# Performance work log

Hardware: AMD Instinct MI355X
Metric: run time of the kernel (lower is better)

## Reference

```python
import jax, jax.numpy as jnp
import numpy as np

N = 100000   # nodes
E = 1600000  # edges
D = 128      # input / hidden feature dim
H = 16       # inner GCN bottleneck (gin default hidden_filters=(16,))
C = 40       # num_classes (ogbn-arxiv)
L = 3        # GCN2 layers
EPS = 1e-5   # hk.BatchNorm default eps


def setup_inputs() -> dict:
    key = jax.random.key(0)
    ks = jax.random.split(key, 8)
    x = jax.random.normal(ks[0], (N, D), jnp.float32)
    vals = jax.random.uniform(ks[1], (E,), jnp.float32)
    row = jnp.sort(jax.random.randint(ks[2], (E,), 0, N, jnp.int32))
    col = jax.random.randint(ks[3], (E,), 0, N, jnp.int32)
    W1 = jax.random.normal(ks[4], (L, D, H), jnp.float32) * 0.1
    b1 = jnp.zeros((L, H), jnp.float32)
    W2 = jax.random.normal(ks[5], (L, H, D), jnp.float32) * 0.1
    b2 = jnp.zeros((L, D), jnp.float32)
    gamma = jnp.ones((L, D), jnp.float32)
    beta = jnp.zeros((L, D), jnp.float32)
    W1f = jax.random.normal(ks[6], (D, H), jnp.float32) * 0.1
    b1f = jnp.zeros((H,), jnp.float32)
    W2f = jax.random.normal(ks[7], (H, C), jnp.float32) * 0.1
    b2f = jnp.zeros((C,), jnp.float32)
    return dict(x=x, vals=vals, W1=W1, b1=b1, W2=W2, b2=b2, gamma=gamma,
                beta=beta, W1f=W1f, b1f=b1f, W2f=W2f, b2f=b2f, row=row, col=col)


def spmm(row, col, vals, h):
    # out[i] = sum_{e: row[e]==i} vals[e] * h[col[e]]  (A @ h, A sparse COO)
    return jax.ops.segment_sum(vals[:, None] * h[col], row,
                               num_segments=N, indices_are_sorted=True)


def gcn_block(x, row, col, vals, w1, c1, w2, c2):
    # inner GCN: GraphConv(16) -> relu -> GraphConv(out); dropout_rate=0 -> identity
    h = spmm(row, col, vals, x @ w1) + c1
    h = jax.nn.relu(h)
    return spmm(row, col, vals, h @ w2) + c2


def reference(x, vals, W1, b1, W2, b2, gamma, beta, W1f, b1f, W2f, b2f, row, col):
    for i in range(L):
        h = gcn_block(x, row, col, vals, W1[i], b1[i], W2[i], b2[i])
        # BatchNorm (training mode: batch stats over node axis)
        mean = jnp.mean(h, axis=0)
        var = jnp.mean(jnp.square(h), axis=0) - jnp.square(mean)
        h = (h - mean) * jax.lax.rsqrt(var + EPS) * gamma[i] + beta[i]
        x = jax.nn.relu(h)
    logits = gcn_block(x, row, col, vals, W1f, b1f, W2f, b2f)
    return logits
```

## Files before the change

### kernel.cpp

```cpp
#include <hip/hip_runtime.h>

#define NN 100000
#define NE 1600000
#define DD 128
#define HH 16
#define CC 40
#define LL 3

typedef int   vi4 __attribute__((ext_vector_type(4)));
typedef float vf4 __attribute__((ext_vector_type(4)));

__device__ __forceinline__ float4 f4fma(float s, float4 w, float4 a) {
    a.x = fmaf(s, w.x, a.x); a.y = fmaf(s, w.y, a.y);
    a.z = fmaf(s, w.z, a.z); a.w = fmaf(s, w.w, a.w);
    return a;
}

__device__ __forceinline__ unsigned short f2bf(float f) {
    unsigned u = __float_as_uint(f);
    unsigned r = u + 0x7fffu + ((u >> 16) & 1u);
    return (unsigned short)(r >> 16);
}
__device__ __forceinline__ unsigned pk2(float a, float b) {
    return (unsigned)f2bf(a) | ((unsigned)f2bf(b) << 16);
}
__device__ __forceinline__ float bflo(unsigned u) { return __uint_as_float(u << 16); }
__device__ __forceinline__ float bfhi(unsigned u) { return __uint_as_float(u & 0xffff0000u); }

__device__ __forceinline__ int permW2(int dw) {
    return (dw >> 2) | ((dw & 3) << 3);
}

__global__ void build_rowptr(const int* __restrict__ row, int* __restrict__ rp) {
    int e = blockIdx.x * 256 + threadIdx.x;
    if (e >= NE) return;
    int r1 = row[e];
    int r0 = (e == 0) ? -1 : row[e - 1];
    for (int i = r0 + 1; i <= r1; i++) rp[i] = e;
    if (e == NE - 1) {
        for (int i = r1 + 1; i <= NN; i++) rp[i] = NE;
    }
}

__global__ void zero_buf(float* __restrict__ s, int n) {
    int i = blockIdx.x * 256 + threadIdx.x;
    if (i < n) s[i] = 0.f;
}

__launch_bounds__(256)
__global__ void gemm_dh_reg(const float* __restrict__ X, const float* __restrict__ W,
                            unsigned* __restrict__ Y) {
    __shared__ float4 Ws[DD * 4];
    int t = threadIdx.x;
    for (int i = t; i < DD * 4; i += 256) Ws[i] = ((const float4*)W)[i];
    __syncthreads();
    int n = blockIdx.x * 256 + t;
    if (n >= NN) return;
    const float4* X4 = (const float4*)(X + (size_t)n * DD);
    float4 y0 = {0,0,0,0}, y1 = {0,0,0,0}, y2 = {0,0,0,0}, y3 = {0,0,0,0};
    #pragma unroll 8
    for (int dc = 0; dc < 32; dc++) {
        float4 xv = X4[dc];
        float xs[4] = {xv.x, xv.y, xv.z, xv.w};
        #pragma unroll
        for (int j = 0; j < 4; j++) {
            int d = dc * 4 + j;
            float xj = xs[j];
            y0 = f4fma(xj, Ws[d * 4 + 0], y0);
            y1 = f4fma(xj, Ws[d * 4 + 1], y1);
            y2 = f4fma(xj, Ws[d * 4 + 2], y2);
            y3 = f4fma(xj, Ws[d * 4 + 3], y3);
        }
    }
    uint4 o0 = {pk2(y0.x, y0.y), pk2(y0.z, y0.w), pk2(y1.x, y1.y), pk2(y1.z, y1.w)};
    uint4 o1 = {pk2(y2.x, y2.y), pk2(y2.z, y2.w), pk2(y3.x, y3.y), pk2(y3.z, y3.w)};
    ((uint4*)Y)[(size_t)n * 2]     = o0;
    ((uint4*)Y)[(size_t)n * 2 + 1] = o1;
}

#define FMA_B(vv, g0, g1, g2, g3)                                                      \
    acc.x = fmaf(vv.x, bflo(g0.x), acc.x); acc.y = fmaf(vv.x, bfhi(g0.x), acc.y);      \
    acc.z = fmaf(vv.x, bflo(g0.y), acc.z); acc.w = fmaf(vv.x, bfhi(g0.y), acc.w);      \
    acc.x = fmaf(vv.y, bflo(g1.x), acc.x); acc.y = fmaf(vv.y, bfhi(g1.x), acc.y);      \
    acc.z = fmaf(vv.y, bflo(g1.y), acc.z); acc.w = fmaf(vv.y, bfhi(g1.y), acc.w);      \
    acc.x = fmaf(vv.z, bflo(g2.x), acc.x); acc.y = fmaf(vv.z, bfhi(g2.x), acc.y);      \
    acc.z = fmaf(vv.z, bflo(g2.y), acc.z); acc.w = fmaf(vv.z, bfhi(g2.y), acc.w);      \
    acc.x = fmaf(vv.w, bflo(g3.x), acc.x); acc.y = fmaf(vv.w, bfhi(g3.x), acc.y);      \
    acc.z = fmaf(vv.w, bflo(g3.y), acc.z); acc.w = fmaf(vv.w, bfhi(g3.y), acc.w);

__device__ __forceinline__ void ldc(const int* __restrict__ col,
                                    const float* __restrict__ vals,
                                    int jb, int s, int e, vi4& c, vf4& v) {
    c = *(const vi4*)(col + jb);
    vf4 w = *(const vf4*)(vals + jb);
    int r = jb - s;
    unsigned deg = (unsigned)(e - s);
    v.x = ((unsigned)(r + 0) < deg) ? w.x : 0.f;
    v.y = ((unsigned)(r + 1) < deg) ? w.y : 0.f;
    v.z = ((unsigned)(r + 2) < deg) ? w.z : 0.f;
    v.w = ((unsigned)(r + 3) < deg) ? w.w : 0.f;
}

template <bool RELU, bool BIAS, bool OBF, bool GRAM, bool FINAL>
__launch_bounds__(256)
__global__ void spmm16(const int* __restrict__ rp, const int* __restrict__ col,
                       const float* __restrict__ vals, const unsigned* __restrict__ hin,
                       const float* __restrict__ bias, void* __restrict__ outv,
                       float* __restrict__ GS, const float* __restrict__ Wf,
                       const float* __restrict__ bf, float* __restrict__ outc) {
    __shared__ float2 Wc[FINAL ? HH * 20 : 1];
    __shared__ float2 Bc[FINAL ? 20 : 1];
    if (FINAL) {
        for (int i = threadIdx.x; i < HH * 20; i += 256) Wc[i] = ((const float2*)Wf)[i];
        if (threadIdx.x < 20) Bc[threadIdx.x] = ((const float2*)bf)[threadIdx.x];
    }
    int node = blockIdx.x * 64 + (threadIdx.x >> 2);
    int f = threadIdx.x & 3;
    bool valid = node < NN;
    if (!GRAM && !FINAL && !valid) return;
    float4 acc = {0, 0, 0, 0};
    if (valid) {
        int s = rp[node], e = rp[node + 1];
        const uint2* h2 = (const uint2*)hin;
        int deg = e - s;
        if (deg > 0) {
            int s0 = s & ~3;
            int B = (e - s0 + 3) >> 2;
            vi4 c2, c0, c1; vf4 v0, v1, v2;
            ldc(col, vals, s0, s, e, c0, v0);
            if (B > 1) ldc(col, vals, s0 + 4, s, e, c1, v1);
            else { c1 = c0; v1 = (vf4){0, 0, 0, 0}; }
            if (B > 2) ldc(col, vals, s0 + 8, s, e, c2, v2);
            else { c2 = c1; v2 = (vf4){0, 0, 0, 0}; }
            uint2 gA0 = h2[(size_t)c0.x * 4 + f], gA1 = h2[(size_t)c0.y * 4 + f];
            uint2 gA2 = h2[(size_t)c0.z * 4 + f], gA3 = h2[(size_t)c0.w * 4 + f];
            uint2 gB0 = h2[(size_t)c1.x * 4 + f], gB1 = h2[(size_t)c1.y * 4 + f];
            uint2 gB2 = h2[(size_t)c1.z * 4 + f], gB3 = h2[(size_t)c1.w * 4 + f];
            for (int b = 0; b < B; b++) {
                vi4 c3; vf4 v3;
                if (b + 3 < B) ldc(col, vals, s0 + ((b + 3) << 2), s, e, c3, v3);
                else { c3 = c2; v3 = (vf4){0, 0, 0, 0}; }
                uint2 gC0 = h2[(size_t)c2.x * 4 + f], gC1 = h2[(size_t)c2.y * 4 + f];
                uint2 gC2 = h2[(size_t)c2.z * 4 + f], gC3 = h2[(size_t)c2.w * 4 + f];
                FMA_B(v0, gA0, gA1, gA2, gA3)
                v0 = v1; v1 = v2; v2 = v3; c2 = c3;
                gA0 = gB0; gA1 = gB1; gA2 = gB2; gA3 = gB3;
                gB0 = gC0; gB1 = gC1; gB2 = gC2; gB3 = gC3;
            }
        }
        if (BIAS) {
            float4 b = ((const float4*)bias)[f];
            acc.x += b.x; acc.y += b.y; acc.z += b.z; acc.w += b.w;
        }
        if (RELU) {
            acc.x = fmaxf(acc.x, 0.f); acc.y = fmaxf(acc.y, 0.f);
            acc.z = fmaxf(acc.z, 0.f); acc.w = fmaxf(acc.w, 0.f);
        }
        if (!FINAL) {
            if (OBF) {
                uint2 o = {pk2(acc.x, acc.y), pk2(acc.z, acc.w)};
                ((uint2*)outv)[(size_t)node * 4 + f] = o;
            } else {
                ((float4*)outv)[(size_t)node * 4 + f] = acc;
            }
        }
    }
    if (GRAM) {
        __shared__ float Us[64 * 20];
        int nl = threadIdx.x >> 2;
        float4 z = valid ? acc : (float4){0, 0, 0, 0};
        ((float4*)&Us[nl * 20])[f] = z;
        __syncthreads();
        int k = threadIdx.x & 15, kp = threadIdx.x >> 4;
        float g = 0.f, s = 0.f;
        for (int n = 0; n < 64; n++) {
            float a = Us[n * 20 + k];
            float b = Us[n * 20 + kp];
            g = fmaf(a, b, g);
            s += a;
        }
        float* gs = GS + (blockIdx.x & 7) * 272;
        atomicAdd(&gs[kp * 16 + k], g);
        if (kp == 0) atomicAdd(&gs[256 + k], s);
    }
    if (FINAL) {
        __shared__ float Us[64 * 20];
        int nl = threadIdx.x >> 2;
        ((float4*)&Us[nl * 20])[f] = acc;
        __syncthreads();
        int p = threadIdx.x & 3;
        int onode = blockIdx.x * 64 + (threadIdx.x >> 2);
        if (onode < NN) {
            float u[16];
            #pragma unroll
            for (int k = 0; k < 16; k++) u[k] = Us[(threadIdx.x >> 2) * 20 + k];
            float2 a5[5];
            #pragma unroll
            for (int i = 0; i < 5; i++) a5[i] = Bc[p * 5 + i];
            #pragma unroll
            for (int k = 0; k < 16; k++) {
                float uk = u[k];
                #pragma unroll
                for (int i = 0; i < 5; i++) {
                    float2 w = Wc[k * 20 + p * 5 + i];
                    a5[i].x = fmaf(uk, w.x, a5[i].x);
                    a5[i].y = fmaf(uk, w.y, a5[i].y);
                }
            }
            float2* O = (float2*)(outc + (size_t)onode * CC) + p * 5;
            #pragma unroll
            for (int i = 0; i < 5; i++) O[i] = a5[i];
        }
    }
}

__launch_bounds__(128)
__global__ void bn_prep(const float* __restrict__ GS, const float* __restrict__ W2,
                        const float* __restrict__ b2, const float* __restrict__ gamma,
                        const float* __restrict__ beta, float* __restrict__ SCSH) {
    __shared__ float Gs[272];
    int t = threadIdx.x;
    for (int i = t; i < 272; i += 128) {
        float a = 0.f;
        #pragma unroll
        for (int c = 0; c < 8; c++) a += GS[c * 272 + i];
        Gs[i] = a;
    }
    __syncthreads();
    int d = t;
    float w[16];
    #pragma unroll
    for (int k = 0; k < 16; k++) w[k] = W2[k * DD + d];
    float sdot = 0.f, quad = 0.f;
    #pragma unroll
    for (int k = 0; k < 16; k++) {
        sdot = fmaf(Gs[256 + k], w[k], sdot);
        float vk = 0.f;
        #pragma unroll
        for (int kp = 0; kp < 16; kp++) vk = fmaf(Gs[k * 16 + kp], w[kp], vk);
        quad = fmaf(w[k], vk, quad);
    }
    float b = b2[d];
    float sumH  = sdot + (float)NN * b;
    float sumsq = quad + 2.f * b * sdot + (float)NN * b * b;
    float mean = sumH * (1.f / NN);
    float var  = sumsq * (1.f / NN) - mean * mean;
    float inv  = rsqrtf(var + 1e-5f);
    float gm = gamma[d] * inv;
    SCSH[d] = gm;
    SCSH[128 + d] = (b - mean) * gm + beta[d];
}

__launch_bounds__(256)
__global__ void fused_mid(const float* __restrict__ U, const float* __restrict__ SCSH,
                          const float* __restrict__ W2, const float* __restrict__ W1n,
                          unsigned* __restrict__ Y) {
    __shared__ float4 W2s[HH * 32];
    __shared__ float4 W1s[DD * 4];
    __shared__ float4 SC4[32], SH4[32];
    int t = threadIdx.x;
    for (int i = t; i < HH * 32; i += 256) {
        int k = i >> 5, dw = i & 31;
        W2s[k * 32 + permW2(dw)] = ((const float4*)W2)[i];
    }
    for (int i = t; i < DD * 4; i += 256) {
        int d = i >> 2, q = i & 3;
        W1s[d * 4 + ((q + (d >> 4)) & 3)] = ((const float4*)W1n)[i];
    }
    if (t < 32) SC4[permW2(t)] = ((const float4*)SCSH)[t];
    else if (t < 64) SH4[permW2(t - 32)] = ((const float4*)SCSH)[t];
    __syncthreads();
    int g = t >> 3, p = t & 7;
    int base = blockIdx.x * 64;
    int n[2]; bool v[2];
    #pragma unroll
    for (int i = 0; i < 2; i++) { n[i] = base + i * 32 + g; v[i] = n[i] < NN; }
    float u[2][16];
    #pragma unroll
    for (int i = 0; i < 2; i++) {
        if (v[i]) {
            const float4* up = (const float4*)(U + (size_t)n[i] * HH);
            float4 a = up[0], b = up[1], c = up[2], d = up[3];
            u[i][0]=a.x; u[i][1]=a.y; u[i][2]=a.z; u[i][3]=a.w;
            u[i][4]=b.x; u[i][5]=b.y; u[i][6]=b.z; u[i][7]=b.w;
            u[i][8]=c.x; u[i][9]=c.y; u[i][10]=c.z; u[i][11]=c.w;
            u[i][12]=d.x; u[i][13]=d.y; u[i][14]=d.z; u[i][15]=d.w;
        } else {
            #pragma unroll
            for (int k = 0; k < 16; k++) u[i][k] = 0.f;
        }
    }
    float4 y[2][4];
    #pragma unroll
    for (int i = 0; i < 2; i++)
        #pragma unroll
        for (int q = 0; q < 4; q++) y[i][q] = {0, 0, 0, 0};
    #pragma unroll
    for (int dqi = 0; dqi < 4; dqi++) {
        int rpos = p + (dqi << 3);
        float4 h[2] = {{0,0,0,0},{0,0,0,0}};
        #pragma unroll
        for (int k = 0; k < 16; k++) {
            float4 w = W2s[k * 32 + rpos];
            h[0] = f4fma(u[0][k], w, h[0]);
            h[1] = f4fma(u[1][k], w, h[1]);
        }
        float4 s4 = SC4[rpos], t4 = SH4[rpos];
        #pragma unroll
        for (int i = 0; i < 2; i++) {
            h[i].x = fmaxf(fmaf(h[i].x, s4.x, t4.x), 0.f);
            h[i].y = fmaxf(fmaf(h[i].y, s4.y, t4.y), 0.f);
            h[i].z = fmaxf(fmaf(h[i].z, s4.z, t4.z), 0.f);
            h[i].w = fmaxf(fmaf(h[i].w, s4.w, t4.w), 0.f);
        }
        int dq = (p << 2) + dqi;
        #pragma unroll
        for (int j = 0; j < 4; j++) {
            int d = (dq << 2) + j;
            float4 w0 = W1s[d * 4 + ((0 + p) & 3)];
            float4 w1 = W1s[d * 4 + ((1 + p) & 3)];
            float4 w2 = W1s[d * 4 + ((2 + p) & 3)];
            float4 w3 = W1s[d * 4 + ((3 + p) & 3)];
            float h0 = j == 0 ? h[0].x : j == 1 ? h[0].y : j == 2 ? h[0].z : h[0].w;
            float h1 = j == 0 ? h[1].x : j == 1 ? h[1].y : j == 2 ? h[1].z : h[1].w;
            y[0][0] = f4fma(h0, w0, y[0][0]); y[0][1] = f4fma(h0, w1, y[0][1]);
            y[0][2] = f4fma(h0, w2, y[0][2]); y[0][3] = f4fma(h0, w3, y[0][3]);
            y[1][0] = f4fma(h1, w0, y[1][0]); y[1][1] = f4fma(h1, w1, y[1][1]);
            y[1][2] = f4fma(h1, w2, y[1][2]); y[1][3] = f4fma(h1, w3, y[1][3]);
        }
    }
    float4 ar[4];
    #pragma unroll
    for (int q = 0; q < 4; q++) {
        float4 z0 = y[0][q], z1 = y[1][q];
        z0.x += __shfl_xor(z0.x, 4); z0.y += __shfl_xor(z0.y, 4);
        z0.z += __shfl_xor(z0.z, 4); z0.w += __shfl_xor(z0.w, 4);
        z1.x += __shfl_xor(z1.x, 4); z1.y += __shfl_xor(z1.y, 4);
        z1.z += __shfl_xor(z1.z, 4); z1.w += __shfl_xor(z1.w, 4);
        ar[q].x = (p & 4) ? z1.x : z0.x;
        ar[q].y = (p & 4) ? z1.y : z0.y;
        ar[q].z = (p & 4) ? z1.z : z0.z;
        ar[q].w = (p & 4) ? z1.w : z0.w;
    }
    float4 br[2];
    #pragma unroll
    for (int q = 0; q < 2; q++) {
        float4 z0 = ar[q], z1 = ar[2 + q];
        z0.x += __shfl_xor(z0.x, 2); z0.y += __shfl_xor(z0.y, 2);
        z0.z += __shfl_xor(z0.z, 2); z0.w += __shfl_xor(z0.w, 2);
        z1.x += __shfl_xor(z1.x, 2); z1.y += __shfl_xor(z1.y, 2);
        z1.z += __shfl_xor(z1.z, 2); z1.w += __shfl_xor(z1.w, 2);
        br[q].x = (p & 2) ? z1.x : z0.x;
        br[q].y = (p & 2) ? z1.y : z0.y;
        br[q].z = (p & 2) ? z1.z : z0.z;
        br[q].w = (p & 2) ? z1.w : z0.w;
    }
    float4 c;
    {
        float4 z0 = br[0], z1 = br[1];
        z0.x += __shfl_xor(z0.x, 1); z0.y += __shfl_xor(z0.y, 1);
        z0.z += __shfl_xor(z0.z, 1); z0.w += __shfl_xor(z0.w, 1);
        z1.x += __shfl_xor(z1.x, 1); z1.y += __shfl_xor(z1.y, 1);
        z1.z += __shfl_xor(z1.z, 1); z1.w += __shfl_xor(z1.w, 1);
        c.x = (p & 1) ? z1.x : z0.x;
        c.y = (p & 1) ? z1.y : z0.y;
        c.z = (p & 1) ? z1.z : z0.z;
        c.w = (p & 1) ? z1.w : z0.w;
    }
    bool vv = (p & 4) ? v[1] : v[0];
    int  nn = (p & 4) ? n[1] : n[0];
    int  q  = p & 3;
    if (vv) {
        uint2 o = {pk2(c.x, c.y), pk2(c.z, c.w)};
        ((uint2*)Y)[(size_t)nn * 4 + q] = o;
    }
}

extern "C" void kernel_launch(void* const* d_in, const int* in_sizes, int n_in,
                              void* d_out, int out_size, void* d_ws, size_t ws_size,
                              hipStream_t stream) {
    const float* x     = (const float*)d_in[0];
    const float* vals  = (const float*)d_in[1];
    const float* W1    = (const float*)d_in[2];
    const float* b1    = (const float*)d_in[3];
    const float* W2    = (const float*)d_in[4];
    const float* b2    = (const float*)d_in[5];
    const float* gamma = (const float*)d_in[6];
    const float* beta  = (const float*)d_in[7];
    const float* W1f   = (const float*)d_in[8];
    const float* b1f   = (const float*)d_in[9];
    const float* W2f   = (const float*)d_in[10];
    const float* b2f   = (const float*)d_in[11];
    const int*   row   = (const int*)d_in[12];
    const int*   col   = (const int*)d_in[13];
    float* out = (float*)d_out;

    char* ws = (char*)d_ws;
    size_t off = 0;
    auto alloc = [&](size_t bytes) -> char* {
        char* p = ws + off;
        off += (bytes + 255) / 256 * 256;
        return p;
    };
    int*      rp   = (int*)     alloc((NN + 1) * sizeof(int));
    float*    GSC  = (float*)   alloc((size_t)LL * 8 * 272 * sizeof(float));
    float*    SCSH = (float*)   alloc(256 * sizeof(float));
    unsigned* Yb   = (unsigned*)alloc((size_t)NN * HH * 2);
    unsigned* Tb   = (unsigned*)alloc((size_t)NN * HH * 2);
    float*    U    = (float*)   alloc((size_t)NN * HH * sizeof(float));

    build_rowptr<<<(NE + 255) / 256, 256, 0, stream>>>(row, rp);
    zero_buf<<<(LL * 8 * 272 + 255) / 256, 256, 0, stream>>>(GSC, LL * 8 * 272);

    gemm_dh_reg<<<(NN + 255) / 256, 256, 0, stream>>>(x, W1, Yb);
    for (int l = 0; l < LL; l++) {
        spmm16<true, true, true, false, false><<<(NN + 63) / 64, 256, 0, stream>>>(
            rp, col, vals, Yb, b1 + l * HH, Tb, nullptr, nullptr, nullptr, nullptr);
        spmm16<false, false, false, true, false><<<(NN + 63) / 64, 256, 0, stream>>>(
            rp, col, vals, Tb, nullptr, U, GSC + (size_t)l * 8 * 272, nullptr, nullptr, nullptr);
        bn_prep<<<1, 128, 0, stream>>>(GSC + (size_t)l * 8 * 272, W2 + l * HH * DD,
                                       b2 + l * DD, gamma + l * DD, beta + l * DD, SCSH);
        const float* W1next = (l < LL - 1) ? (W1 + (l + 1) * DD * HH) : W1f;
        fused_mid<<<(NN + 63) / 64, 256, 0, stream>>>(U, SCSH, W2 + l * HH * DD, W1next, Yb);
    }
    spmm16<true, true, true, false, false><<<(NN + 63) / 64, 256, 0, stream>>>(
        rp, col, vals, Yb, b1f, Tb, nullptr, nullptr, nullptr, nullptr);
    spmm16<false, false, false, false, true><<<(NN + 63) / 64, 256, 0, stream>>>(
        rp, col, vals, Tb, nullptr, nullptr, nullptr, W2f, b2f, out);
}
```

Before: 370.5 us.

## Bin nodes by SpMM trip count and process them in permuted order

Adds a preprocessing pass (count, prefix, scatter) that groups nodes into 16 bins by their padded neighbor-chunk trip count and builds a permutation. Each SpMM launch then maps threads to nodes through this permutation, so nodes in the same wavefront have similar degree and fewer lanes sit idle in the edge loop. In exchange it adds several small kernel launches, including a serial per-bin prefix scan over all blocks. Row-pointer reads and output writes also become scattered rather than contiguous.

```diff
diff --git a/kernel.cpp b/kernel.cpp
--- a/kernel.cpp
+++ b/kernel.cpp
@@ -6,6 +6,7 @@
 #define HH 16
 #define CC 40
 #define LL 3
+#define NBINB ((NN + 255) / 256)
 
 typedef int   vi4 __attribute__((ext_vector_type(4)));
 typedef float vf4 __attribute__((ext_vector_type(4)));
@@ -45,6 +46,58 @@
 __global__ void zero_buf(float* __restrict__ s, int n) {
     int i = blockIdx.x * 256 + threadIdx.x;
     if (i < n) s[i] = 0.f;
+}
+
+__device__ __forceinline__ int trip_bin(const int* __restrict__ rp, int n) {
+    int s = rp[n], e = rp[n + 1];
+    return min(15, (e - (s & ~3) + 3) >> 2);
+}
+
+__global__ void bin_count(const int* __restrict__ rp, int* __restrict__ bh,
+                          int* __restrict__ gh) {
+    __shared__ int lh[16];
+    int t = threadIdx.x;
+    if (t < 16) lh[t] = 0;
+    __syncthreads();
+    int n = blockIdx.x * 256 + t;
+    if (n < NN) atomicAdd(&lh[trip_bin(rp, n)], 1);
+    __syncthreads();
+    if (t < 16) {
+        bh[blockIdx.x * 16 + t] = lh[t];
+        atomicAdd(&gh[t], lh[t]);
+    }
+}
+
+__global__ void bin_prefix(const int* __restrict__ gh, const int* __restrict__ bh,
+                           int* __restrict__ bbase) {
+    __shared__ int gbase[16];
+    if (threadIdx.x == 0) {
+        int a = 0;
+        for (int i = 0; i < 16; i++) { gbase[i] = a; a += gh[i]; }
+    }
+    __syncthreads();
+    if (threadIdx.x < 16) {
+        int bin = threadIdx.x;
+        int a = gbase[bin];
+        for (int b = 0; b < NBINB; b++) {
+            bbase[b * 16 + bin] = a;
+            a += bh[b * 16 + bin];
+        }
+    }
+}
+
+__global__ void bin_scatter(const int* __restrict__ rp, const int* __restrict__ bbase,
+                            int* __restrict__ perm) {
+    __shared__ int cnt[16];
+    int t = threadIdx.x;
+    if (t < 16) cnt[t] = 0;
+    __syncthreads();
+    int n = blockIdx.x * 256 + t;
+    if (n < NN) {
+        int B = trip_bin(rp, n);
+        int r = atomicAdd(&cnt[B], 1);
+        perm[bbase[blockIdx.x * 16 + B] + r] = n;
+    }
 }
 
 __launch_bounds__(256)
@@ -107,16 +160,18 @@
                        const float* __restrict__ vals, const unsigned* __restrict__ hin,
                        const float* __restrict__ bias, void* __restrict__ outv,
                        float* __restrict__ GS, const float* __restrict__ Wf,
-                       const float* __restrict__ bf, float* __restrict__ outc) {
+                       const float* __restrict__ bf, float* __restrict__ outc,
+                       const int* __restrict__ perm) {
     __shared__ float2 Wc[FINAL ? HH * 20 : 1];
     __shared__ float2 Bc[FINAL ? 20 : 1];
     if (FINAL) {
         for (int i = threadIdx.x; i < HH * 20; i += 256) Wc[i] = ((const float2*)Wf)[i];
         if (threadIdx.x < 20) Bc[threadIdx.x] = ((const float2*)bf)[threadIdx.x];
     }
-    int node = blockIdx.x * 64 + (threadIdx.x >> 2);
+    int lid = blockIdx.x * 64 + (threadIdx.x >> 2);
     int f = threadIdx.x & 3;
-    bool valid = node < NN;
+    bool valid = lid < NN;
+    int node = valid ? perm[lid] : 0;
     if (!GRAM && !FINAL && !valid) return;
     float4 acc = {0, 0, 0, 0};
     if (valid) {
@@ -189,8 +244,7 @@
         ((float4*)&Us[nl * 20])[f] = acc;
         __syncthreads();
         int p = threadIdx.x & 3;
-        int onode = blockIdx.x * 64 + (threadIdx.x >> 2);
-        if (onode < NN) {
+        if (valid) {
             float u[16];
             #pragma unroll
             for (int k = 0; k < 16; k++) u[k] = Us[(threadIdx.x >> 2) * 20 + k];
@@ -207,7 +261,7 @@
                     a5[i].y = fmaf(uk, w.y, a5[i].y);
                 }
             }
-            float2* O = (float2*)(outc + (size_t)onode * CC) + p * 5;
+            float2* O = (float2*)(outc + (size_t)node * CC) + p * 5;
             #pragma unroll
             for (int i = 0; i < 5; i++) O[i] = a5[i];
         }
@@ -402,29 +456,38 @@
         off += (bytes + 255) / 256 * 256;
         return p;
     };
-    int*      rp   = (int*)     alloc((NN + 1) * sizeof(int));
-    float*    GSC  = (float*)   alloc((size_t)LL * 8 * 272 * sizeof(float));
-    float*    SCSH = (float*)   alloc(256 * sizeof(float));
-    unsigned* Yb   = (unsigned*)alloc((size_t)NN * HH * 2);
-    unsigned* Tb   = (unsigned*)alloc((size_t)NN * HH * 2);
-    float*    U    = (float*)   alloc((size_t)NN * HH * sizeof(float));
+    int*      rp    = (int*)     alloc((NN + 1) * sizeof(int));
+    float*    GSC   = (float*)   alloc((size_t)LL * 8 * 272 * sizeof(float));
+    float*    SCSH  = (float*)   alloc(256 * sizeof(float));
+    unsigned* Yb    = (unsigned*)alloc((size_t)NN * HH * 2);
+    unsigned* Tb    = (unsigned*)alloc((size_t)NN * HH * 2);
+    float*    U     = (float*)   alloc((size_t)NN * HH * sizeof(float));
+    int*      bh    = (int*)     alloc((size_t)NBINB * 16 * sizeof(int));
+    int*      bbase = (int*)     alloc((size_t)NBINB * 16 * sizeof(int));
+    int*      gh    = (int*)     alloc(16 * sizeof(int));
+    int*      perm  = (int*)     alloc((size_t)NN * sizeof(int));
 
     build_rowptr<<<(NE + 255) / 256, 256, 0, stream>>>(row, rp);
     zero_buf<<<(LL * 8 * 272 + 255) / 256, 256, 0, stream>>>(GSC, LL * 8 * 272);
+    zero_buf<<<1, 256, 0, stream>>>((float*)gh, 16);
+
+    bin_count<<<NBINB, 256, 0, stream>>>(rp, bh, gh);
+    bin_prefix<<<1, 256, 0, stream>>>(gh, bh, bbase);
+    bin_scatter<<<NBINB, 256, 0, stream>>>(rp, bbase, perm);
 
     gemm_dh_reg<<<(NN + 255) / 256, 256, 0, stream>>>(x, W1, Yb);
     for (int l = 0; l < LL; l++) {
         spmm16<true, true, true, false, false><<<(NN + 63) / 64, 256, 0, stream>>>(
-            rp, col, vals, Yb, b1 + l * HH, Tb, nullptr, nullptr, nullptr, nullptr);
+            rp, col, vals, Yb, b1 + l * HH, Tb, nullptr, nullptr, nullptr, nullptr, perm);
         spmm16<false, false, false, true, false><<<(NN + 63) / 64, 256, 0, stream>>>(
-            rp, col, vals, Tb, nullptr, U, GSC + (size_t)l * 8 * 272, nullptr, nullptr, nullptr);
+            rp, col, vals, Tb, nullptr, U, GSC + (size_t)l * 8 * 272, nullptr, nullptr, nullptr, perm);
         bn_prep<<<1, 128, 0, stream>>>(GSC + (size_t)l * 8 * 272, W2 + l * HH * DD,
                                        b2 + l * DD, gamma + l * DD, beta + l * DD, SCSH);
         const float* W1next = (l < LL - 1) ? (W1 + (l + 1) * DD * HH) : W1f;
         fused_mid<<<(NN + 63) / 64, 256, 0, stream>>>(U, SCSH, W2 + l * HH * DD, W1next, Yb);
     }
     spmm16<true, true, true, false, false><<<(NN + 63) / 64, 256, 0, stream>>>(
-        rp, col, vals, Yb, b1f, Tb, nullptr, nullptr, nullptr, nullptr);
+        rp, col, vals, Yb, b1f, Tb, nullptr, nullptr, nullptr, nullptr, perm);
     spmm16<false, false, false, false, true><<<(NN + 63) / 64, 256, 0, stream>>>(
-        rp, col, vals, Tb, nullptr, nullptr, nullptr, W2f, b2f, out);
-}
+        rp, col, vals, Tb, nullptr, nullptr, nullptr, W2f, b2f, out, perm);
+}
```

Result: slower. 435.2 us (+17.4%).

## Sort nodes by trip count within each 64-node block and use nontemporal loads for col and vals

Applied to the files above, without the earlier changes.

Adds a local_sort kernel that reorders nodes within each 64-node block by their number of 4-edge chunks. Every spmm16 launch then reads its node index through that permutation, so the lanes of a wavefront handle rows of similar length and spend less time diverging. Loads of col and vals are also made nontemporal, to keep that streamed edge data from evicting the gathered feature rows from cache. The cost is one extra launch, an extra indirection per node, and scattered output writes. The GRAM and non-final paths write U and Tb through the permuted node index in code not shown here, so correctness depends on those writes also using node.

```diff
diff --git a/kernel.cpp b/kernel.cpp
--- a/kernel.cpp
+++ b/kernel.cpp
@@ -45,6 +45,29 @@
 __global__ void zero_buf(float* __restrict__ s, int n) {
     int i = blockIdx.x * 256 + threadIdx.x;
     if (i < n) s[i] = 0.f;
+}
+
+__device__ __forceinline__ int trip_bin(const int* __restrict__ rp, int n) {
+    int s = rp[n], e = rp[n + 1];
+    return (e - (s & ~3) + 3) >> 2;
+}
+
+__global__ void local_sort(const int* __restrict__ rp, int* __restrict__ perm) {
+    __shared__ int Bs[64];
+    int t = threadIdx.x;
+    int base = blockIdx.x * 64;
+    int n = base + t;
+    int B = (n < NN) ? trip_bin(rp, n) : -1;
+    Bs[t] = B;
+    __syncthreads();
+    if (n < NN) {
+        int rank = 0;
+        for (int j = 0; j < 64; j++) {
+            int Bj = Bs[j];
+            rank += (Bj > B) || (Bj == B && j < t);
+        }
+        perm[base + rank] = n;
+    }
 }
 
 __launch_bounds__(256)
@@ -91,8 +114,8 @@
 __device__ __forceinline__ void ldc(const int* __restrict__ col,
                                     const float* __restrict__ vals,
                                     int jb, int s, int e, vi4& c, vf4& v) {
-    c = *(const vi4*)(col + jb);
-    vf4 w = *(const vf4*)(vals + jb);
+    c = __builtin_nontemporal_load((const vi4*)(col + jb));
+    vf4 w = __builtin_nontemporal_load((const vf4*)(vals + jb));
     int r = jb - s;
     unsigned deg = (unsigned)(e - s);
     v.x = ((unsigned)(r + 0) < deg) ? w.x : 0.f;
@@ -107,16 +130,18 @@
                        const float* __restrict__ vals, const unsigned* __restrict__ hin,
                        const float* __restrict__ bias, void* __restrict__ outv,
                        float* __restrict__ GS, const float* __restrict__ Wf,
-                       const float* __restrict__ bf, float* __restrict__ outc) {
+                       const float* __restrict__ bf, float* __restrict__ outc,
+                       const int* __restrict__ perm) {
     __shared__ float2 Wc[FINAL ? HH * 20 : 1];
     __shared__ float2 Bc[FINAL ? 20 : 1];
     if (FINAL) {
         for (int i = threadIdx.x; i < HH * 20; i += 256) Wc[i] = ((const float2*)Wf)[i];
         if (threadIdx.x < 20) Bc[threadIdx.x] = ((const float2*)bf)[threadIdx.x];
     }
-    int node = blockIdx.x * 64 + (threadIdx.x >> 2);
+    int lid = blockIdx.x * 64 + (threadIdx.x >> 2);
     int f = threadIdx.x & 3;
-    bool valid = node < NN;
+    bool valid = lid < NN;
+    int node = valid ? perm[lid] : 0;
     if (!GRAM && !FINAL && !valid) return;
     float4 acc = {0, 0, 0, 0};
     if (valid) {
@@ -189,8 +214,7 @@
         ((float4*)&Us[nl * 20])[f] = acc;
         __syncthreads();
         int p = threadIdx.x & 3;
-        int onode = blockIdx.x * 64 + (threadIdx.x >> 2);
-        if (onode < NN) {
+        if (valid) {
             float u[16];
             #pragma unroll
             for (int k = 0; k < 16; k++) u[k] = Us[(threadIdx.x >> 2) * 20 + k];
@@ -207,7 +231,7 @@
                     a5[i].y = fmaf(uk, w.y, a5[i].y);
                 }
             }
-            float2* O = (float2*)(outc + (size_t)onode * CC) + p * 5;
+            float2* O = (float2*)(outc + (size_t)node * CC) + p * 5;
             #pragma unroll
             for (int i = 0; i < 5; i++) O[i] = a5[i];
         }
@@ -408,23 +432,25 @@
     unsigned* Yb   = (unsigned*)alloc((size_t)NN * HH * 2);
     unsigned* Tb   = (unsigned*)alloc((size_t)NN * HH * 2);
     float*    U    = (float*)   alloc((size_t)NN * HH * sizeof(float));
+    int*      perm = (int*)     alloc((size_t)((NN + 63) / 64 * 64) * sizeof(int));
 
     build_rowptr<<<(NE + 255) / 256, 256, 0, stream>>>(row, rp);
     zero_buf<<<(LL * 8 * 272 + 255) / 256, 256, 0, stream>>>(GSC, LL * 8 * 272);
+    local_sort<<<(NN + 63) / 64, 64, 0, stream>>>(rp, perm);
 
     gemm_dh_reg<<<(NN + 255) / 256, 256, 0, stream>>>(x, W1, Yb);
     for (int l = 0; l < LL; l++) {
         spmm16<true, true, true, false, false><<<(NN + 63) / 64, 256, 0, stream>>>(
-            rp, col, vals, Yb, b1 + l * HH, Tb, nullptr, nullptr, nullptr, nullptr);
+            rp, col, vals, Yb, b1 + l * HH, Tb, nullptr, nullptr, nullptr, nullptr, perm);
         spmm16<false, false, false, true, false><<<(NN + 63) / 64, 256, 0, stream>>>(
-            rp, col, vals, Tb, nullptr, U, GSC + (size_t)l * 8 * 272, nullptr, nullptr, nullptr);
+            rp, col, vals, Tb, nullptr, U, GSC + (size_t)l * 8 * 272, nullptr, nullptr, nullptr, perm);
         bn_prep<<<1, 128, 0, stream>>>(GSC + (size_t)l * 8 * 272, W2 + l * HH * DD,
                                        b2 + l * DD, gamma + l * DD, beta + l * DD, SCSH);
         const float* W1next = (l < LL - 1) ? (W1 + (l + 1) * DD * HH) : W1f;
         fused_mid<<<(NN + 63) / 64, 256, 0, stream>>>(U, SCSH, W2 + l * HH * DD, W1next, Yb);
     }
     spmm16<true, true, true, false, false><<<(NN + 63) / 64, 256, 0, stream>>>(
-        rp, col, vals, Yb, b1f, Tb, nullptr, nullptr, nullptr, nullptr);
+        rp, col, vals, Yb, b1f, Tb, nullptr, nullptr, nullptr, nullptr, perm);
     spmm16<false, false, false, false, true><<<(NN + 63) / 64, 256, 0, stream>>>(
-        rp, col, vals, Tb, nullptr, nullptr, nullptr, W2f, b2f, out);
-}
+        rp, col, vals, Tb, nullptr, nullptr, nullptr, W2f, b2f, out, perm);
+}
```

Result: slower. 447.2 us (+20.7%).

## Stage block's col/vals slice in LDS and deepen gather prefetch to four batches

Applied to the files above, without the earlier changes.

Each block of 64 nodes now loads its contiguous range of column indices and edge values into shared memory with coalesced vector loads before the per-node loop. It falls back to global memory past the 2048-entry capacity. The software pipeline also goes from three to four batches of neighbour gathers in flight, to hide more gather latency. The cost is about 16 KB of extra LDS per block, which may lower occupancy, plus a block-wide barrier and more registers.

```diff
diff --git a/kernel.cpp b/kernel.cpp
--- a/kernel.cpp
+++ b/kernel.cpp
@@ -88,18 +88,9 @@
     acc.x = fmaf(vv.w, bflo(g3.x), acc.x); acc.y = fmaf(vv.w, bfhi(g3.x), acc.y);      \
     acc.z = fmaf(vv.w, bflo(g3.y), acc.z); acc.w = fmaf(vv.w, bfhi(g3.y), acc.w);
 
-__device__ __forceinline__ void ldc(const int* __restrict__ col,
-                                    const float* __restrict__ vals,
-                                    int jb, int s, int e, vi4& c, vf4& v) {
-    c = *(const vi4*)(col + jb);
-    vf4 w = *(const vf4*)(vals + jb);
-    int r = jb - s;
-    unsigned deg = (unsigned)(e - s);
-    v.x = ((unsigned)(r + 0) < deg) ? w.x : 0.f;
-    v.y = ((unsigned)(r + 1) < deg) ? w.y : 0.f;
-    v.z = ((unsigned)(r + 2) < deg) ? w.z : 0.f;
-    v.w = ((unsigned)(r + 3) < deg) ? w.w : 0.f;
-}
+#define GATH(g0, g1, g2, g3, cc)                                \
+    g0 = h2[(size_t)cc.x * 4 + f]; g1 = h2[(size_t)cc.y * 4 + f]; \
+    g2 = h2[(size_t)cc.z * 4 + f]; g3 = h2[(size_t)cc.w * 4 + f];
 
 template <bool RELU, bool BIAS, bool OBF, bool GRAM, bool FINAL>
 __launch_bounds__(256)
@@ -108,44 +99,76 @@
                        const float* __restrict__ bias, void* __restrict__ outv,
                        float* __restrict__ GS, const float* __restrict__ Wf,
                        const float* __restrict__ bf, float* __restrict__ outc) {
+    __shared__ int   Lc[2048];
+    __shared__ float Lv[2048];
     __shared__ float2 Wc[FINAL ? HH * 20 : 1];
     __shared__ float2 Bc[FINAL ? 20 : 1];
     if (FINAL) {
         for (int i = threadIdx.x; i < HH * 20; i += 256) Wc[i] = ((const float2*)Wf)[i];
         if (threadIdx.x < 20) Bc[threadIdx.x] = ((const float2*)bf)[threadIdx.x];
     }
-    int node = blockIdx.x * 64 + (threadIdx.x >> 2);
+    int base = blockIdx.x * 64;
+    int w0 = rp[base] & ~3;
+    int w1 = rp[min(base + 64, NN)];
+    int S4 = min((w1 - w0) & ~3, 2048);
+    for (int i = threadIdx.x; i < (S4 >> 2); i += 256) {
+        ((vi4*)Lc)[i] = ((const vi4*)(col + w0))[i];
+        ((vf4*)Lv)[i] = ((const vf4*)(vals + w0))[i];
+    }
+    __syncthreads();
+
+    int node = base + (threadIdx.x >> 2);
     int f = threadIdx.x & 3;
     bool valid = node < NN;
-    if (!GRAM && !FINAL && !valid) return;
     float4 acc = {0, 0, 0, 0};
     if (valid) {
         int s = rp[node], e = rp[node + 1];
         const uint2* h2 = (const uint2*)hin;
-        int deg = e - s;
+        unsigned deg = (unsigned)(e - s);
         if (deg > 0) {
             int s0 = s & ~3;
             int B = (e - s0 + 3) >> 2;
-            vi4 c2, c0, c1; vf4 v0, v1, v2;
-            ldc(col, vals, s0, s, e, c0, v0);
-            if (B > 1) ldc(col, vals, s0 + 4, s, e, c1, v1);
-            else { c1 = c0; v1 = (vf4){0, 0, 0, 0}; }
-            if (B > 2) ldc(col, vals, s0 + 8, s, e, c2, v2);
-            else { c2 = c1; v2 = (vf4){0, 0, 0, 0}; }
-            uint2 gA0 = h2[(size_t)c0.x * 4 + f], gA1 = h2[(size_t)c0.y * 4 + f];
-            uint2 gA2 = h2[(size_t)c0.z * 4 + f], gA3 = h2[(size_t)c0.w * 4 + f];
-            uint2 gB0 = h2[(size_t)c1.x * 4 + f], gB1 = h2[(size_t)c1.y * 4 + f];
-            uint2 gB2 = h2[(size_t)c1.z * 4 + f], gB3 = h2[(size_t)c1.w * 4 + f];
+            int li = s0 - w0;
+            auto LDB = [&](int b, vi4& C, vf4& V) {
+                int off = li + (b << 2);
+                vi4 c; vf4 w;
+                if (off + 4 <= S4) {
+                    c = *(const vi4*)&Lc[off];
+                    w = *(const vf4*)&Lv[off];
+                } else {
+                    c = *(const vi4*)(col + w0 + off);
+                    w = *(const vf4*)(vals + w0 + off);
+                }
+                int r = (w0 + off) - s;
+                V.x = ((unsigned)(r + 0) < deg) ? w.x : 0.f;
+                V.y = ((unsigned)(r + 1) < deg) ? w.y : 0.f;
+                V.z = ((unsigned)(r + 2) < deg) ? w.z : 0.f;
+                V.w = ((unsigned)(r + 3) < deg) ? w.w : 0.f;
+                C = c;
+            };
+            vi4 cA, cB, cC, cD; vf4 vA, vB, vC, vD;
+            LDB(0, cA, vA);
+            if (B > 1) LDB(1, cB, vB); else { cB = cA; vB = (vf4){0,0,0,0}; }
+            if (B > 2) LDB(2, cC, vC); else { cC = cB; vC = (vf4){0,0,0,0}; }
+            if (B > 3) LDB(3, cD, vD); else { cD = cC; vD = (vf4){0,0,0,0}; }
+            uint2 gA0, gA1, gA2, gA3, gB0, gB1, gB2, gB3;
+            uint2 gC0, gC1, gC2, gC3, gD0, gD1, gD2, gD3;
+            GATH(gA0, gA1, gA2, gA3, cA)
+            GATH(gB0, gB1, gB2, gB3, cB)
+            GATH(gC0, gC1, gC2, gC3, cC)
+            GATH(gD0, gD1, gD2, gD3, cD)
             for (int b = 0; b < B; b++) {
-                vi4 c3; vf4 v3;
-                if (b + 3 < B) ldc(col, vals, s0 + ((b + 3) << 2), s, e, c3, v3);
-                else { c3 = c2; v3 = (vf4){0, 0, 0, 0}; }
-                uint2 gC0 = h2[(size_t)c2.x * 4 + f], gC1 = h2[(size_t)c2.y * 4 + f];
-                uint2 gC2 = h2[(size_t)c2.z * 4 + f], gC3 = h2[(size_t)c2.w * 4 + f];
-                FMA_B(v0, gA0, gA1, gA2, gA3)
-                v0 = v1; v1 = v2; v2 = v3; c2 = c3;
+                vi4 cN; vf4 vN;
+                if (b + 4 < B) LDB(b + 4, cN, vN);
+                else { cN = cD; vN = (vf4){0,0,0,0}; }
+                uint2 gN0, gN1, gN2, gN3;
+                GATH(gN0, gN1, gN2, gN3, cN)
+                FMA_B(vA, gA0, gA1, gA2, gA3)
+                vA = vB; vB = vC; vC = vD; vD = vN; cD = cN;
                 gA0 = gB0; gA1 = gB1; gA2 = gB2; gA3 = gB3;
                 gB0 = gC0; gB1 = gC1; gB2 = gC2; gB3 = gC3;
+                gC0 = gD0; gC1 = gD1; gC2 = gD2; gC3 = gD3;
+                gD0 = gN0; gD1 = gN1; gD2 = gN2; gD3 = gN3;
             }
         }
         if (BIAS) {
@@ -189,8 +212,7 @@
         ((float4*)&Us[nl * 20])[f] = acc;
         __syncthreads();
         int p = threadIdx.x & 3;
-        int onode = blockIdx.x * 64 + (threadIdx.x >> 2);
-        if (onode < NN) {
+        if (valid) {
             float u[16];
             #pragma unroll
             for (int k = 0; k < 16; k++) u[k] = Us[(threadIdx.x >> 2) * 20 + k];
@@ -207,7 +229,7 @@
                     a5[i].y = fmaf(uk, w.y, a5[i].y);
                 }
             }
-            float2* O = (float2*)(outc + (size_t)onode * CC) + p * 5;
+            float2* O = (float2*)(outc + (size_t)node * CC) + p * 5;
             #pragma unroll
             for (int i = 0; i < 5; i++) O[i] = a5[i];
         }
```

After: 379.3 us. 2.4% more time.
